# Optimization experiments

Hardware: AMD Instinct MI355X
Metric: run time of the kernel (lower is better)

The kernel has to match this reference:

```python
import jax, jax.numpy as jnp
import numpy as np

DIM, HEADS, NB_FEATURES = 512, 8, 64
HEAD_DIM = DIM // HEADS


def setup_inputs() -> dict:
    key = jax.random.key(0)
    k_x, k_qkv, k_pm, k_wp, k_bp = jax.random.split(key, 5)
    B, N = 8, 4096
    x = jax.random.normal(k_x, (B, N, DIM), dtype=jnp.float32)
    # to_qkv: Linear(dim, 3*dim, bias=False) -> apply as x @ w_qkv
    w_qkv = jax.random.normal(k_qkv, (DIM, 3 * DIM), dtype=jnp.float32) * (1.0 / np.sqrt(DIM))
    # random projection buffer [H, D, F]
    proj_mat = jax.random.normal(k_pm, (HEADS, HEAD_DIM, NB_FEATURES), dtype=jnp.float32)
    # output projection Linear(dim, dim) with bias
    w_proj = jax.random.normal(k_wp, (DIM, DIM), dtype=jnp.float32) * (1.0 / np.sqrt(DIM))
    b_proj = jax.random.normal(k_bp, (DIM,), dtype=jnp.float32) * 0.01
    return {"x": x, "w_qkv": w_qkv, "proj_mat": proj_mat, "w_proj": w_proj, "b_proj": b_proj}


def _phi(t, proj_mat):
    # t: [B,N,H,D], proj_mat: [H,D,F] -> [B,N,H,F]
    return jax.nn.elu(jnp.einsum('bnhd,hdf->bnhf', t, proj_mat)) + 1.0


def reference(x, w_qkv, proj_mat, w_proj, b_proj):
    B, N, dim = x.shape
    H, D = HEADS, dim // HEADS
    qkv = x @ w_qkv  # [B,N,3*dim]
    q, k, v = jnp.split(qkv, 3, axis=-1)
    q = q.reshape(B, N, H, D)
    k = k.reshape(B, N, H, D)
    v = v.reshape(B, N, H, D)
    q_phi = _phi(q, proj_mat)  # [B,N,H,F]
    k_phi = _phi(k, proj_mat)  # [B,N,H,F]
    kv = jnp.einsum('bnhf,bnhd->bhfd', k_phi, v)  # [B,H,F,D]
    z = 1.0 / jnp.einsum('bnhf,bhf->bnh', q_phi, k_phi.sum(axis=1))  # [B,N,H]
    out = jnp.einsum('bnhf,bhfd,bnh->bnhd', q_phi, kv, z)  # [B,N,H,D]
    out = out.reshape(B, N, H * D)
    return out @ w_proj + b_proj
```

## Files before the change

kernel.cpp:

```cpp
#include <hip/hip_runtime.h>
#include <hip/hip_bf16.h>

typedef __bf16 bf16_t;
typedef __bf16 bf16x4 __attribute__((ext_vector_type(4)));
typedef __bf16 bf16x8 __attribute__((ext_vector_type(8)));
typedef float f32x4 __attribute__((ext_vector_type(4)));

__device__ __forceinline__ void gload16(const void* g, void* l) {
  __builtin_amdgcn_global_load_lds((const __attribute__((address_space(1))) void*)g,
                                   (__attribute__((address_space(3))) void*)l, 16, 0, 0);
}

__global__ __launch_bounds__(256) void prep_qk(const float* __restrict__ w_qkv,
                                               const float* __restrict__ proj,
                                               bf16_t* __restrict__ WeffT) {
  const int half = blockIdx.x >> 3, h = blockIdx.x & 7;
  const int i0 = blockIdx.y * 64;
  __shared__ float P[64 * 64];
  __shared__ float Wt[64][65];
  const int t = threadIdx.x;
  #pragma unroll
  for (int r = 0; r < 16; ++r) P[t + 256 * r] = proj[(size_t)h * 4096 + t + 256 * r];
  #pragma unroll
  for (int r = 0; r < 16; ++r) {
    const int idx = t + 256 * r;
    Wt[idx >> 6][idx & 63] =
        w_qkv[(size_t)(i0 + (idx >> 6)) * 1536 + half * 512 + h * 64 + (idx & 63)];
  }
  __syncthreads();
  const int i = t & 63, fg = t >> 6;
  for (int f = fg; f < 64; f += 4) {
    float s = 0.f;
    #pragma unroll
    for (int d = 0; d < 64; ++d) s += Wt[i][d] * P[d * 64 + f];
    WeffT[(size_t)(half * 512 + h * 64 + f) * 512 + i0 + i] = (bf16_t)s;
  }
}

__global__ __launch_bounds__(256) void prep_v(const float* __restrict__ w_qkv,
                                              bf16_t* __restrict__ WeffT) {
  __shared__ bf16_t tile[32][33];
  const int i0 = blockIdx.x * 32, n0 = blockIdx.y * 32;
  const int tn = threadIdx.x & 31, ti = threadIdx.x >> 5;
  #pragma unroll
  for (int p = 0; p < 4; ++p) {
    const int i = ti + p * 8;
    tile[i][tn] = (bf16_t)w_qkv[(size_t)(i0 + i) * 1536 + 1024 + n0 + tn];
  }
  __syncthreads();
  #pragma unroll
  for (int p = 0; p < 4; ++p) {
    const int n = ti + p * 8;
    WeffT[(size_t)(1024 + n0 + n) * 512 + i0 + tn] = tile[tn][n];
  }
}

__global__ __launch_bounds__(256) void cast_x(const f32x4* __restrict__ x,
                                              bf16x4* __restrict__ xb, int n4) {
  int i = blockIdx.x * 256 + threadIdx.x;
  if (i < n4) {
    f32x4 v = x[i];
    bf16x4 o;
    #pragma unroll
    for (int j = 0; j < 4; ++j) o[j] = (bf16_t)v[j];
    xb[i] = o;
  }
}

template <int MODE>
__global__ __launch_bounds__(256) void gemm_pq(const bf16_t* __restrict__ P,
                                               const bf16_t* __restrict__ Q,
                                               bf16_t* __restrict__ Cq,
                                               bf16_t* __restrict__ kT,
                                               bf16_t* __restrict__ vT,
                                               float* __restrict__ Cout,
                                               const float* __restrict__ bias,
                                               size_t sP, size_t sQ) {
  constexpr int K = 512;
  constexpr int BK = 64;
  __shared__ alignas(16) bf16_t Ps[128 * BK];
  __shared__ alignas(16) bf16_t Qs[128 * BK];
  const int t = threadIdx.x;
  const int z = blockIdx.z;
  const bf16_t* Pp = P + (size_t)z * sP;
  const bf16_t* Qp = Q + (size_t)z * sQ;
  const int w = t >> 6, l = t & 63;
  const int wr = w >> 1, wc = w & 1;
  const int lrow = l & 15, lkb = l >> 4;
  const size_t pm0 = (size_t)blockIdx.x * 128;
  const size_t qn0 = (size_t)blockIdx.y * 128;

  const int st_r = l >> 3;
  const int st_c = ((l & 7) ^ st_r) * 8;
  size_t p_src[4], q_src[4];
  #pragma unroll
  for (int c = 0; c < 4; ++c) {
    const int q8 = c * 4 + w;
    p_src[c] = (pm0 + q8 * 8 + st_r) * (size_t)K + st_c;
    q_src[c] = (qn0 + q8 * 8 + st_r) * (size_t)K + st_c;
  }

  f32x4 acc[4][4];
  #pragma unroll
  for (int m = 0; m < 4; ++m)
    #pragma unroll
    for (int n = 0; n < 4; ++n) acc[m][n] = f32x4{0.f, 0.f, 0.f, 0.f};

  const char* PsB = (const char*)Ps;
  const char* QsB = (const char*)Qs;

  for (int kt = 0; kt < K; kt += BK) {
    #pragma unroll
    for (int c = 0; c < 4; ++c) {
      const int q8 = c * 4 + w;
      gload16(Pp + p_src[c] + kt, (char*)Ps + q8 * 1024);
      gload16(Qp + q_src[c] + kt, (char*)Qs + q8 * 1024);
    }
    __syncthreads();
    bf16x8 pf[4][2], qf[4][2];
    #pragma unroll
    for (int m = 0; m < 4; ++m) {
      const int r = wr * 64 + m * 16 + lrow;
      #pragma unroll
      for (int kk = 0; kk < 2; ++kk) {
        const int kb = lkb + kk * 4;
        pf[m][kk] = *(const bf16x8*)(PsB + r * 128 + (((kb ^ (r & 7)) & 7) << 4));
      }
    }
    #pragma unroll
    for (int n = 0; n < 4; ++n) {
      const int r = wc * 64 + n * 16 + lrow;
      #pragma unroll
      for (int kk = 0; kk < 2; ++kk) {
        const int kb = lkb + kk * 4;
        qf[n][kk] = *(const bf16x8*)(QsB + r * 128 + (((kb ^ (r & 7)) & 7) << 4));
      }
    }
    #pragma unroll
    for (int m = 0; m < 4; ++m)
      #pragma unroll
      for (int n = 0; n < 4; ++n) {
        acc[m][n] = __builtin_amdgcn_mfma_f32_16x16x32_bf16(pf[m][0], qf[n][0], acc[m][n], 0, 0, 0);
        acc[m][n] = __builtin_amdgcn_mfma_f32_16x16x32_bf16(pf[m][1], qf[n][1], acc[m][n], 0, 0, 0);
      }
    __syncthreads();
  }

  #pragma unroll
  for (int m = 0; m < 4; ++m) {
    #pragma unroll
    for (int n = 0; n < 4; ++n) {
      const int prow0 = (int)pm0 + wr * 64 + m * 16 + lkb * 4;
      const int qrow  = (int)qn0 + wc * 64 + n * 16 + lrow;
      if (MODE == 0) {
        bf16x4 o;
        #pragma unroll
        for (int j = 0; j < 4; ++j) {
          float v = acc[m][n][j];
          o[j] = (bf16_t)(v > 0.f ? v + 1.f : __expf(v));
        }
        *(bf16x4*)&Cq[(size_t)qrow * 512 + prow0] = o;
      } else if (MODE == 1) {
        const int feat = qrow;
        const int half = feat >> 9, h = (feat >> 6) & 7, f = feat & 63;
        const int b = prow0 >> 12, nn = prow0 & 4095;
        bf16x4 o;
        #pragma unroll
        for (int j = 0; j < 4; ++j) {
          float v = acc[m][n][j];
          if (half == 0) v = v > 0.f ? v + 1.f : __expf(v);
          o[j] = (bf16_t)v;
        }
        bf16_t* dst = (half ? vT : kT) + ((size_t)((b * 8 + h) * 64 + f)) * 4096 + nn;
        *(bf16x4*)dst = o;
      } else {
        f32x4 v = acc[m][n];
        #pragma unroll
        for (int j = 0; j < 4; ++j) v[j] += bias[prow0 + j];
        *(f32x4*)&Cout[((size_t)z * 4096 + qrow) * 512 + prow0] = v;
      }
    }
  }
}

__global__ __launch_bounds__(256) void kv_mfma(const bf16_t* __restrict__ kT,
                                               const bf16_t* __restrict__ vT,
                                               float* __restrict__ kv,
                                               float* __restrict__ ksum) {
  const int bh = blockIdx.x;
  const int nbase = blockIdx.y * 512;
  __shared__ alignas(16) bf16_t Ks[64 * 64];
  __shared__ alignas(16) bf16_t Vs[64 * 64];
  const int t = threadIdx.x, w = t >> 6, l = t & 63;
  const int wr = w >> 1, wc = w & 1;
  const int lrow = l & 15, lkb = l >> 4;
  const int st_r = l >> 3;
  const int st_c = ((l & 7) ^ st_r) * 8;
  const bf16_t* Kp = kT + (size_t)bh * 64 * 4096;
  const bf16_t* Vp = vT + (size_t)bh * 64 * 4096;
  const char* KsB = (const char*)Ks;
  const char* VsB = (const char*)Vs;

  f32x4 acc[2][2];
  #pragma unroll
  for (int m = 0; m < 2; ++m)
    #pragma unroll
    for (int n = 0; n < 2; ++n) acc[m][n] = f32x4{0.f, 0.f, 0.f, 0.f};
  float ksf[2] = {0.f, 0.f};

  for (int st = 0; st < 8; ++st) {
    const int nb = nbase + st * 64;
    #pragma unroll
    for (int c = 0; c < 2; ++c) {
      const int q8 = w * 2 + c;
      gload16(Kp + (size_t)(q8 * 8 + st_r) * 4096 + nb + st_c, (char*)Ks + q8 * 1024);
      gload16(Vp + (size_t)(q8 * 8 + st_r) * 4096 + nb + st_c, (char*)Vs + q8 * 1024);
    }
    __syncthreads();
    bf16x8 af[2][2], bf[2][2];
    #pragma unroll
    for (int m = 0; m < 2; ++m) {
      const int r = wr * 32 + m * 16 + lrow;
      #pragma unroll
      for (int kk = 0; kk < 2; ++kk) {
        const int kb = lkb + kk * 4;
        af[m][kk] = *(const bf16x8*)(KsB + r * 128 + (((kb ^ (r & 7)) & 7) << 4));
      }
    }
    #pragma unroll
    for (int n = 0; n < 2; ++n) {
      const int r = wc * 32 + n * 16 + lrow;
      #pragma unroll
      for (int kk = 0; kk < 2; ++kk) {
        const int kb = lkb + kk * 4;
        bf[n][kk] = *(const bf16x8*)(VsB + r * 128 + (((kb ^ (r & 7)) & 7) << 4));
      }
    }
    #pragma unroll
    for (int m = 0; m < 2; ++m)
      #pragma unroll
      for (int n = 0; n < 2; ++n) {
        acc[m][n] = __builtin_amdgcn_mfma_f32_16x16x32_bf16(af[m][0], bf[n][0], acc[m][n], 0, 0, 0);
        acc[m][n] = __builtin_amdgcn_mfma_f32_16x16x32_bf16(af[m][1], bf[n][1], acc[m][n], 0, 0, 0);
      }
    if (wc == 0) {
      #pragma unroll
      for (int m = 0; m < 2; ++m)
        #pragma unroll
        for (int kk = 0; kk < 2; ++kk)
          #pragma unroll
          for (int j = 0; j < 8; ++j) ksf[m] += (float)af[m][kk][j];
    }
    __syncthreads();
  }

  float* kvp = kv + (size_t)bh * 4096;
  #pragma unroll
  for (int m = 0; m < 2; ++m)
    #pragma unroll
    for (int n = 0; n < 2; ++n)
      #pragma unroll
      for (int j = 0; j < 4; ++j)
        atomicAdd(&kvp[(wr * 32 + m * 16 + lkb * 4 + j) * 64 + wc * 32 + n * 16 + lrow],
                  acc[m][n][j]);
  if (wc == 0) {
    #pragma unroll
    for (int m = 0; m < 2; ++m) {
      float s = ksf[m];
      s += __shfl_xor(s, 16);
      s += __shfl_xor(s, 32);
      if (l < 16) atomicAdd(&ksum[(size_t)bh * 64 + wr * 32 + m * 16 + l], s);
    }
  }
}

__global__ __launch_bounds__(256) void w2_kernel(const float* __restrict__ kv,
                                                 const float* __restrict__ w_proj,
                                                 bf16_t* __restrict__ W2T) {
  const int bh = blockIdx.x, b = bh >> 3, h = bh & 7;
  const int j0 = blockIdx.y * 64;
  const int t = threadIdx.x;
  __shared__ float kvs[64][64];
  __shared__ float wps[64][64];
  const float* kvp = kv + (size_t)bh * 4096;
  #pragma unroll
  for (int i = 0; i < 16; ++i) ((float*)kvs)[t + 256 * i] = kvp[t + 256 * i];
  {
    const int d = t >> 2, c16 = (t & 3) * 16;
    const float* src = w_proj + (size_t)(h * 64 + d) * 512 + j0 + c16;
    #pragma unroll
    for (int j = 0; j < 16; ++j) wps[d][c16 + j] = src[j];
  }
  __syncthreads();
  const int fq = t >> 4, jq = t & 15;
  float acc[4][4] = {};
  for (int d = 0; d < 64; ++d) {
    float kf[4], wj[4];
    #pragma unroll
    for (int i = 0; i < 4; ++i) kf[i] = kvs[fq * 4 + i][d];
    #pragma unroll
    for (int i = 0; i < 4; ++i) wj[i] = wps[d][jq * 4 + i];
    #pragma unroll
    for (int i = 0; i < 4; ++i)
      #pragma unroll
      for (int j = 0; j < 4; ++j) acc[i][j] += kf[i] * wj[j];
  }
  #pragma unroll
  for (int j = 0; j < 4; ++j)
    #pragma unroll
    for (int i = 0; i < 4; ++i)
      W2T[((size_t)b * 512 + j0 + jq * 4 + j) * 512 + h * 64 + fq * 4 + i] = (bf16_t)acc[i][j];
}

__global__ __launch_bounds__(256) void zq_kernel(const bf16_t* __restrict__ qphi,
                                                 const float* __restrict__ ksum,
                                                 bf16_t* __restrict__ zq) {
  const int row = blockIdx.x * 4 + (threadIdx.x >> 6);
  const int l = threadIdx.x & 63;
  const int b = row >> 12;
  const int h = l >> 3, f8 = (l & 7) * 8;
  const bf16_t* src = qphi + (size_t)row * 512 + h * 64 + f8;
  bf16x8 v = *(const bf16x8*)src;
  const float* ks = ksum + ((size_t)b * 8 + h) * 64 + f8;
  float part = 0.f;
  float vf[8];
  #pragma unroll
  for (int j = 0; j < 8; ++j) { vf[j] = (float)v[j]; part += vf[j] * ks[j]; }
  part += __shfl_xor(part, 1);
  part += __shfl_xor(part, 2);
  part += __shfl_xor(part, 4);
  const float z = 1.f / part;
  bf16x8 o;
  #pragma unroll
  for (int j = 0; j < 8; ++j) o[j] = (bf16_t)(vf[j] * z);
  *(bf16x8*)(zq + (size_t)row * 512 + h * 64 + f8) = o;
}

extern "C" void kernel_launch(void* const* d_in, const int* in_sizes, int n_in,
                              void* d_out, int out_size, void* d_ws, size_t ws_size,
                              hipStream_t stream) {
  const float* x      = (const float*)d_in[0];
  const float* w_qkv  = (const float*)d_in[1];
  const float* proj   = (const float*)d_in[2];
  const float* w_proj = (const float*)d_in[3];
  const float* b_proj = (const float*)d_in[4];
  float* out = (float*)d_out;
  char* ws = (char*)d_ws;

  bf16_t* x_bf  = (bf16_t*)(ws + 0);
  bf16_t* WeffT = (bf16_t*)(ws + 33554432);
  bf16_t* q_phi = (bf16_t*)(ws + 35127296);
  bf16_t* kT    = (bf16_t*)(ws + 68681728);
  bf16_t* vT    = (bf16_t*)(ws + 102236160);
  float*  kv    = (float*)(ws + 135790592);
  float*  ksum  = (float*)(ws + 136839168);
  bf16_t* W2T   = (bf16_t*)(ws + 136855552);
  bf16_t* zq    = (bf16_t*)(ws + 141049856);

  prep_qk<<<dim3(16, 8), 256, 0, stream>>>(w_qkv, proj, WeffT);
  prep_v<<<dim3(16, 16), 256, 0, stream>>>(w_qkv, WeffT);
  cast_x<<<16384, 256, 0, stream>>>((const f32x4*)x, (bf16x4*)x_bf, 4194304);
  gemm_pq<0><<<dim3(4, 256, 1), 256, 0, stream>>>(WeffT, x_bf, q_phi, nullptr, nullptr,
                                                  nullptr, nullptr, 0, 0);
  gemm_pq<1><<<dim3(256, 8, 1), 256, 0, stream>>>(x_bf, WeffT + 512 * 512, nullptr, kT, vT,
                                                  nullptr, nullptr, 0, 0);
  hipMemsetAsync(kv, 0, 1048576 + 16384, stream);
  kv_mfma<<<dim3(64, 8), 256, 0, stream>>>(kT, vT, kv, ksum);
  w2_kernel<<<dim3(64, 8), 256, 0, stream>>>(kv, w_proj, W2T);
  zq_kernel<<<8192, 256, 0, stream>>>(q_phi, ksum, zq);
  gemm_pq<2><<<dim3(4, 32, 8), 256, 0, stream>>>(W2T, zq, nullptr, nullptr, nullptr, out,
                                                 b_proj, (size_t)512 * 512,
                                                 (size_t)4096 * 512);
}
```

Measured before the change: 200.2 us.

## Double-buffer GEMM and kv tiles, merge QKV GEMMs, stage epilogues through LDS

The two QKV projection GEMMs are merged into one kernel launch whose flat block index is swizzled across XCDs. The GEMM and kv K-loops now double-buffer LDS tiles so the next tile's global-to-LDS load overlaps the current MFMA work, which removes one barrier per iteration. Epilogues write results through a swizzled LDS staging buffer so global stores become coalesced 16-byte rows instead of scattered 8-byte pieces. In exchange the GEMMs use 64KB of LDS per block, which may lower occupancy.

```diff
diff --git a/kernel.cpp b/kernel.cpp
--- a/kernel.cpp
+++ b/kernel.cpp
@@ -67,37 +67,33 @@
   }
 }
 
-template <int MODE>
-__global__ __launch_bounds__(256) void gemm_pq(const bf16_t* __restrict__ P,
-                                               const bf16_t* __restrict__ Q,
-                                               bf16_t* __restrict__ Cq,
-                                               bf16_t* __restrict__ kT,
-                                               bf16_t* __restrict__ vT,
-                                               float* __restrict__ Cout,
-                                               const float* __restrict__ bias,
-                                               size_t sP, size_t sQ) {
-  constexpr int K = 512;
-  constexpr int BK = 64;
-  __shared__ alignas(16) bf16_t Ps[128 * BK];
-  __shared__ alignas(16) bf16_t Qs[128 * BK];
-  const int t = threadIdx.x;
-  const int z = blockIdx.z;
-  const bf16_t* Pp = P + (size_t)z * sP;
-  const bf16_t* Qp = Q + (size_t)z * sQ;
-  const int w = t >> 6, l = t & 63;
+__global__ __launch_bounds__(256) void gemm_qkv(const bf16_t* __restrict__ x_bf,
+                                                const bf16_t* __restrict__ WeffT,
+                                                bf16_t* __restrict__ q_phi,
+                                                bf16_t* __restrict__ kT,
+                                                bf16_t* __restrict__ vT) {
+  constexpr int K = 512, BK = 64;
+  __shared__ alignas(16) char smem[65536];
+  const int t = threadIdx.x, w = t >> 6, l = t & 63;
+  const int hw = blockIdx.x;
+  const int bid = (hw & 7) * 384 + (hw >> 3);
+  const int tok_blk = bid / 12, cb = bid % 12;
+  const size_t tok0 = (size_t)tok_blk * 128;
+  const bool qpath = (cb < 4);
+  const bf16_t* Pp = qpath ? (WeffT + (size_t)cb * 128 * 512) : (x_bf + tok0 * 512);
+  const bf16_t* Qp = qpath ? (x_bf + tok0 * 512)
+                           : (WeffT + (size_t)(512 + (cb - 4) * 128) * 512);
+
   const int wr = w >> 1, wc = w & 1;
   const int lrow = l & 15, lkb = l >> 4;
-  const size_t pm0 = (size_t)blockIdx.x * 128;
-  const size_t qn0 = (size_t)blockIdx.y * 128;
-
   const int st_r = l >> 3;
   const int st_c = ((l & 7) ^ st_r) * 8;
   size_t p_src[4], q_src[4];
   #pragma unroll
   for (int c = 0; c < 4; ++c) {
     const int q8 = c * 4 + w;
-    p_src[c] = (pm0 + q8 * 8 + st_r) * (size_t)K + st_c;
-    q_src[c] = (qn0 + q8 * 8 + st_r) * (size_t)K + st_c;
+    p_src[c] = (size_t)(q8 * 8 + st_r) * K + st_c;
+    q_src[c] = (size_t)(q8 * 8 + st_r) * K + st_c;
   }
 
   f32x4 acc[4][4];
@@ -106,17 +102,27 @@
     #pragma unroll
     for (int n = 0; n < 4; ++n) acc[m][n] = f32x4{0.f, 0.f, 0.f, 0.f};
 
-  const char* PsB = (const char*)Ps;
-  const char* QsB = (const char*)Qs;
-
+  #pragma unroll
+  for (int c = 0; c < 4; ++c) {
+    const int q8 = c * 4 + w;
+    gload16(Pp + p_src[c], smem + q8 * 1024);
+    gload16(Qp + q_src[c], smem + 16384 + q8 * 1024);
+  }
+  __syncthreads();
+
+  int cur = 0;
   for (int kt = 0; kt < K; kt += BK) {
-    #pragma unroll
-    for (int c = 0; c < 4; ++c) {
-      const int q8 = c * 4 + w;
-      gload16(Pp + p_src[c] + kt, (char*)Ps + q8 * 1024);
-      gload16(Qp + q_src[c] + kt, (char*)Qs + q8 * 1024);
-    }
-    __syncthreads();
+    if (kt + BK < K) {
+      char* nb = smem + (cur ^ 1) * 32768;
+      #pragma unroll
+      for (int c = 0; c < 4; ++c) {
+        const int q8 = c * 4 + w;
+        gload16(Pp + p_src[c] + kt + BK, nb + q8 * 1024);
+        gload16(Qp + q_src[c] + kt + BK, nb + 16384 + q8 * 1024);
+      }
+    }
+    const char* PsB = smem + cur * 32768;
+    const char* QsB = PsB + 16384;
     bf16x8 pf[4][2], qf[4][2];
     #pragma unroll
     for (int m = 0; m < 4; ++m) {
@@ -144,41 +150,42 @@
         acc[m][n] = __builtin_amdgcn_mfma_f32_16x16x32_bf16(pf[m][1], qf[n][1], acc[m][n], 0, 0, 0);
       }
     __syncthreads();
-  }
-
-  #pragma unroll
-  for (int m = 0; m < 4; ++m) {
-    #pragma unroll
-    for (int n = 0; n < 4; ++n) {
-      const int prow0 = (int)pm0 + wr * 64 + m * 16 + lkb * 4;
-      const int qrow  = (int)qn0 + wc * 64 + n * 16 + lrow;
-      if (MODE == 0) {
-        bf16x4 o;
-        #pragma unroll
-        for (int j = 0; j < 4; ++j) {
-          float v = acc[m][n][j];
-          o[j] = (bf16_t)(v > 0.f ? v + 1.f : __expf(v));
-        }
-        *(bf16x4*)&Cq[(size_t)qrow * 512 + prow0] = o;
-      } else if (MODE == 1) {
-        const int feat = qrow;
-        const int half = feat >> 9, h = (feat >> 6) & 7, f = feat & 63;
-        const int b = prow0 >> 12, nn = prow0 & 4095;
-        bf16x4 o;
-        #pragma unroll
-        for (int j = 0; j < 4; ++j) {
-          float v = acc[m][n][j];
-          if (half == 0) v = v > 0.f ? v + 1.f : __expf(v);
-          o[j] = (bf16_t)v;
-        }
-        bf16_t* dst = (half ? vT : kT) + ((size_t)((b * 8 + h) * 64 + f)) * 4096 + nn;
-        *(bf16x4*)dst = o;
-      } else {
-        f32x4 v = acc[m][n];
-        #pragma unroll
-        for (int j = 0; j < 4; ++j) v[j] += bias[prow0 + j];
-        *(f32x4*)&Cout[((size_t)z * 4096 + qrow) * 512 + prow0] = v;
-      }
+    cur ^= 1;
+  }
+
+  bf16_t* ep = (bf16_t*)smem;
+  const bool doElu = qpath || (cb < 8);
+  #pragma unroll
+  for (int n = 0; n < 4; ++n) {
+    const int qc = wc * 64 + n * 16 + lrow;
+    #pragma unroll
+    for (int m = 0; m < 4; ++m) {
+      const int pr0 = wr * 64 + m * 16 + lkb * 4;
+      bf16x4 o;
+      #pragma unroll
+      for (int j = 0; j < 4; ++j) {
+        float v = acc[m][n][j];
+        if (doElu) v = v > 0.f ? v + 1.f : __expf(v);
+        o[j] = (bf16_t)v;
+      }
+      const int u = pr0 >> 3;
+      *(bf16x4*)((char*)ep + qc * 256 + ((u ^ (qc & 15)) << 4) + (pr0 & 7) * 2) = o;
+    }
+  }
+  __syncthreads();
+  #pragma unroll
+  for (int i = 0; i < 8; ++i) {
+    const int flat = i * 256 + t;
+    const int qc2 = flat >> 4, u2 = flat & 15;
+    bf16x8 vv = *(const bf16x8*)((char*)ep + qc2 * 256 + ((u2 ^ (qc2 & 15)) << 4));
+    if (qpath) {
+      *(bf16x8*)&q_phi[(tok0 + qc2) * 512 + cb * 128 + u2 * 8] = vv;
+    } else {
+      const int f512 = (cb - 4) * 128 + qc2;
+      bf16_t* dst = (f512 < 512 ? kT + ((size_t)(tok0 >> 12) * 512 + f512) * 4096
+                                : vT + ((size_t)(tok0 >> 12) * 512 + (f512 - 512)) * 4096) +
+                    (tok0 & 4095) + u2 * 8;
+      *(bf16x8*)dst = vv;
     }
   }
 }
@@ -189,8 +196,7 @@
                                                float* __restrict__ ksum) {
   const int bh = blockIdx.x;
   const int nbase = blockIdx.y * 512;
-  __shared__ alignas(16) bf16_t Ks[64 * 64];
-  __shared__ alignas(16) bf16_t Vs[64 * 64];
+  __shared__ alignas(16) char smem[32768];
   const int t = threadIdx.x, w = t >> 6, l = t & 63;
   const int wr = w >> 1, wc = w & 1;
   const int lrow = l & 15, lkb = l >> 4;
@@ -198,8 +204,6 @@
   const int st_c = ((l & 7) ^ st_r) * 8;
   const bf16_t* Kp = kT + (size_t)bh * 64 * 4096;
   const bf16_t* Vp = vT + (size_t)bh * 64 * 4096;
-  const char* KsB = (const char*)Ks;
-  const char* VsB = (const char*)Vs;
 
   f32x4 acc[2][2];
   #pragma unroll
@@ -208,15 +212,28 @@
     for (int n = 0; n < 2; ++n) acc[m][n] = f32x4{0.f, 0.f, 0.f, 0.f};
   float ksf[2] = {0.f, 0.f};
 
+  #pragma unroll
+  for (int c = 0; c < 2; ++c) {
+    const int q8 = w * 2 + c;
+    gload16(Kp + (size_t)(q8 * 8 + st_r) * 4096 + nbase + st_c, smem + q8 * 1024);
+    gload16(Vp + (size_t)(q8 * 8 + st_r) * 4096 + nbase + st_c, smem + 8192 + q8 * 1024);
+  }
+  __syncthreads();
+
+  int cur = 0;
   for (int st = 0; st < 8; ++st) {
-    const int nb = nbase + st * 64;
-    #pragma unroll
-    for (int c = 0; c < 2; ++c) {
-      const int q8 = w * 2 + c;
-      gload16(Kp + (size_t)(q8 * 8 + st_r) * 4096 + nb + st_c, (char*)Ks + q8 * 1024);
-      gload16(Vp + (size_t)(q8 * 8 + st_r) * 4096 + nb + st_c, (char*)Vs + q8 * 1024);
-    }
-    __syncthreads();
+    if (st < 7) {
+      char* nb = smem + (cur ^ 1) * 16384;
+      const int nb2 = nbase + (st + 1) * 64;
+      #pragma unroll
+      for (int c = 0; c < 2; ++c) {
+        const int q8 = w * 2 + c;
+        gload16(Kp + (size_t)(q8 * 8 + st_r) * 4096 + nb2 + st_c, nb + q8 * 1024);
+        gload16(Vp + (size_t)(q8 * 8 + st_r) * 4096 + nb2 + st_c, nb + 8192 + q8 * 1024);
+      }
+    }
+    const char* KsB = smem + cur * 16384;
+    const char* VsB = KsB + 8192;
     bf16x8 af[2][2], bf[2][2];
     #pragma unroll
     for (int m = 0; m < 2; ++m) {
@@ -252,6 +269,7 @@
           for (int j = 0; j < 8; ++j) ksf[m] += (float)af[m][kk][j];
     }
     __syncthreads();
+    cur ^= 1;
   }
 
   float* kvp = kv + (size_t)bh * 4096;
@@ -336,6 +354,116 @@
   *(bf16x8*)(zq + (size_t)row * 512 + h * 64 + f8) = o;
 }
 
+__global__ __launch_bounds__(256) void gemm_out(const bf16_t* __restrict__ W2T,
+                                                const bf16_t* __restrict__ zq,
+                                                float* __restrict__ Cout,
+                                                const float* __restrict__ bias) {
+  constexpr int K = 512, BK = 64;
+  __shared__ alignas(16) char smem[65536];
+  const int t = threadIdx.x, w = t >> 6, l = t & 63;
+  const int hw = blockIdx.x;
+  const int bid = (hw & 7) * 128 + (hw >> 3);
+  const int z = bid >> 7;
+  const int rem = bid & 127;
+  const int qblk = rem >> 2, pblk = rem & 3;
+  const size_t tok0 = (size_t)qblk * 128;
+  const int pj0 = pblk * 128;
+  const bf16_t* Pp = W2T + ((size_t)z * 512 + pj0) * 512;
+  const bf16_t* Qp = zq + ((size_t)z * 4096 + tok0) * 512;
+
+  const int wr = w >> 1, wc = w & 1;
+  const int lrow = l & 15, lkb = l >> 4;
+  const int st_r = l >> 3;
+  const int st_c = ((l & 7) ^ st_r) * 8;
+
+  f32x4 acc[4][4];
+  #pragma unroll
+  for (int m = 0; m < 4; ++m)
+    #pragma unroll
+    for (int n = 0; n < 4; ++n) acc[m][n] = f32x4{0.f, 0.f, 0.f, 0.f};
+
+  #pragma unroll
+  for (int c = 0; c < 4; ++c) {
+    const int q8 = c * 4 + w;
+    gload16(Pp + (size_t)(q8 * 8 + st_r) * K + st_c, smem + q8 * 1024);
+    gload16(Qp + (size_t)(q8 * 8 + st_r) * K + st_c, smem + 16384 + q8 * 1024);
+  }
+  __syncthreads();
+
+  int cur = 0;
+  for (int kt = 0; kt < K; kt += BK) {
+    if (kt + BK < K) {
+      char* nb = smem + (cur ^ 1) * 32768;
+      #pragma unroll
+      for (int c = 0; c < 4; ++c) {
+        const int q8 = c * 4 + w;
+        gload16(Pp + (size_t)(q8 * 8 + st_r) * K + kt + BK + st_c, nb + q8 * 1024);
+        gload16(Qp + (size_t)(q8 * 8 + st_r) * K + kt + BK + st_c, nb + 16384 + q8 * 1024);
+      }
+    }
+    const char* PsB = smem + cur * 32768;
+    const char* QsB = PsB + 16384;
+    bf16x8 pf[4][2], qf[4][2];
+    #pragma unroll
+    for (int m = 0; m < 4; ++m) {
+      const int r = wr * 64 + m * 16 + lrow;
+      #pragma unroll
+      for (int kk = 0; kk < 2; ++kk) {
+        const int kb = lkb + kk * 4;
+        pf[m][kk] = *(const bf16x8*)(PsB + r * 128 + (((kb ^ (r & 7)) & 7) << 4));
+      }
+    }
+    #pragma unroll
+    for (int n = 0; n < 4; ++n) {
+      const int r = wc * 64 + n * 16 + lrow;
+      #pragma unroll
+      for (int kk = 0; kk < 2; ++kk) {
+        const int kb = lkb + kk * 4;
+        qf[n][kk] = *(const bf16x8*)(QsB + r * 128 + (((kb ^ (r & 7)) & 7) << 4));
+      }
+    }
+    #pragma unroll
+    for (int m = 0; m < 4; ++m)
+      #pragma unroll
+      for (int n = 0; n < 4; ++n) {
+        acc[m][n] = __builtin_amdgcn_mfma_f32_16x16x32_bf16(pf[m][0], qf[n][0], acc[m][n], 0, 0, 0);
+        acc[m][n] = __builtin_amdgcn_mfma_f32_16x16x32_bf16(pf[m][1], qf[n][1], acc[m][n], 0, 0, 0);
+      }
+    __syncthreads();
+    cur ^= 1;
+  }
+
+  float* ep = (float*)smem;
+  #pragma unroll
+  for (int p = 0; p < 2; ++p) {
+    if (p) __syncthreads();
+    #pragma unroll
+    for (int nn2 = 0; nn2 < 2; ++nn2) {
+      const int n = p * 2 + nn2;
+      const int r6 = wc * 32 + (n & 1) * 16 + lrow;
+      #pragma unroll
+      for (int m = 0; m < 4; ++m) {
+        const int pr0 = wr * 64 + m * 16 + lkb * 4;
+        f32x4 v = acc[m][n];
+        const f32x4 bv = *(const f32x4*)&bias[pj0 + pr0];
+        #pragma unroll
+        for (int j = 0; j < 4; ++j) v[j] += bv[j];
+        const int u = pr0 >> 2;
+        *(f32x4*)((char*)ep + r6 * 512 + ((u ^ (r6 & 31)) << 4)) = v;
+      }
+    }
+    __syncthreads();
+    #pragma unroll
+    for (int i = 0; i < 8; ++i) {
+      const int flat = i * 256 + t;
+      const int r6 = flat >> 5, u2 = flat & 31;
+      f32x4 v = *(const f32x4*)((char*)ep + r6 * 512 + ((u2 ^ (r6 & 31)) << 4));
+      const int qc = (r6 >> 5) * 64 + p * 32 + (r6 & 31);
+      *(f32x4*)&Cout[((size_t)z * 4096 + tok0 + qc) * 512 + pj0 + u2 * 4] = v;
+    }
+  }
+}
+
 extern "C" void kernel_launch(void* const* d_in, const int* in_sizes, int n_in,
                               void* d_out, int out_size, void* d_ws, size_t ws_size,
                               hipStream_t stream) {
@@ -360,15 +488,10 @@
   prep_qk<<<dim3(16, 8), 256, 0, stream>>>(w_qkv, proj, WeffT);
   prep_v<<<dim3(16, 16), 256, 0, stream>>>(w_qkv, WeffT);
   cast_x<<<16384, 256, 0, stream>>>((const f32x4*)x, (bf16x4*)x_bf, 4194304);
-  gemm_pq<0><<<dim3(4, 256, 1), 256, 0, stream>>>(WeffT, x_bf, q_phi, nullptr, nullptr,
-                                                  nullptr, nullptr, 0, 0);
-  gemm_pq<1><<<dim3(256, 8, 1), 256, 0, stream>>>(x_bf, WeffT + 512 * 512, nullptr, kT, vT,
-                                                  nullptr, nullptr, 0, 0);
+  gemm_qkv<<<3072, 256, 0, stream>>>(x_bf, WeffT, q_phi, kT, vT);
   hipMemsetAsync(kv, 0, 1048576 + 16384, stream);
   kv_mfma<<<dim3(64, 8), 256, 0, stream>>>(kT, vT, kv, ksum);
   w2_kernel<<<dim3(64, 8), 256, 0, stream>>>(kv, w_proj, W2T);
   zq_kernel<<<8192, 256, 0, stream>>>(q_phi, ksum, zq);
-  gemm_pq<2><<<dim3(4, 32, 8), 256, 0, stream>>>(W2T, zq, nullptr, nullptr, nullptr, out,
-                                                 b_proj, (size_t)512 * 512,
-                                                 (size_t)4096 * 512);
-}
+  gemm_out<<<1024, 256, 0, stream>>>(W2T, zq, out, b_proj);
+}
```

After: 184.2 us. -8.0%, faster.
